# Kernel tuning notes

Hardware: AMD Instinct MI355X
Metric: run time of the kernel (lower is better)

Reference implementation:

```python
import jax, jax.numpy as jnp
import numpy as np

B, S, D, H, FF = 2, 4096, 512, 8, 2048
HD = D // H
EPS = 1e-5


def setup_inputs() -> dict:
    key = jax.random.key(0)
    ks = jax.random.split(key, 14)
    init = lambda k, shape: jax.random.normal(k, shape, dtype=jnp.float32) * 0.02
    return {
        "x": jax.random.normal(ks[0], (B, S, D), dtype=jnp.float32),
        "Wq": init(ks[1], (D, D)), "bq": jnp.zeros((D,), jnp.float32),
        "Wk": init(ks[2], (D, D)), "bk": jnp.zeros((D,), jnp.float32),
        "Wv": init(ks[3], (D, D)), "bv": jnp.zeros((D,), jnp.float32),
        "Wo": init(ks[4], (D, D)), "bo": jnp.zeros((D,), jnp.float32),
        "W1": init(ks[5], (D, FF)), "b1": jnp.zeros((FF,), jnp.float32),
        "W2": init(ks[6], (FF, D)), "b2": jnp.zeros((D,), jnp.float32),
        "g1": jnp.ones((D,), jnp.float32), "beta1": jnp.zeros((D,), jnp.float32),
        "g2": jnp.ones((D,), jnp.float32), "beta2": jnp.zeros((D,), jnp.float32),
    }


def layer_norm(x, g, b):
    mu = jnp.mean(x, axis=-1, keepdims=True)
    var = jnp.mean(jnp.square(x - mu), axis=-1, keepdims=True)
    return (x - mu) * jax.lax.rsqrt(var + EPS) * g + b


def reference(x, Wq, bq, Wk, bk, Wv, bv, Wo, bo, W1, b1, W2, b2, g1, beta1, g2, beta2):
    # --- pre-LN self-attention block ---
    residual = x
    h = layer_norm(x, g1, beta1)
    # project and split heads: [B, H, S, HD]
    q = (h @ Wq + bq).reshape(B, S, H, HD).transpose(0, 2, 1, 3)
    k = (h @ Wk + bk).reshape(B, S, H, HD).transpose(0, 2, 1, 3)
    v = (h @ Wv + bv).reshape(B, S, H, HD).transpose(0, 2, 1, 3)
    scale = HD ** -0.5
    scores = jnp.einsum('bhqd,bhkd->bhqk', q, k) * scale  # [B,H,S,S] materialized
    attn = jax.nn.softmax(scores, axis=-1)
    ctx = jnp.einsum('bhqk,bhkd->bhqd', attn, v)
    ctx = ctx.transpose(0, 2, 1, 3).reshape(B, S, D)
    attn_out = ctx @ Wo + bo
    x = residual + attn_out  # dropout p=0.0 -> identity
    # --- pre-LN FFN block ---
    residual = x
    h = layer_norm(x, g2, beta2)
    h = jax.nn.gelu(h @ W1 + b1, approximate=False)  # nn.GELU default = exact erf
    h = h @ W2 + b2
    x = residual + h
    return (x, attn)
```

## Files before the change

kernel.cpp:

```cpp
#include <hip/hip_runtime.h>
#include <hip/hip_bf16.h>

#define B_ 2
#define S_ 4096
#define D_ 512
#define H_ 8
#define HD_ 64
#define FF_ 2048
#define NT_ (B_*S_)
#define EPS_ 1e-5f

typedef __attribute__((ext_vector_type(8))) short bf16x8;
typedef __attribute__((ext_vector_type(4))) float f32x4;
typedef __attribute__((ext_vector_type(4))) unsigned int u32x4;

__device__ __forceinline__ short f2bf(float f){
  __hip_bfloat16 h = __float2bfloat16(f);
  return __builtin_bit_cast(short, h);
}
__device__ __forceinline__ float bf2f(short s){
  return __bfloat162float(__builtin_bit_cast(__hip_bfloat16, s));
}
__device__ __forceinline__ unsigned pack2(float lo, float hi){
  return ((unsigned)(unsigned short)f2bf(hi) << 16) | (unsigned short)f2bf(lo);
}
__device__ __forceinline__ void load8(const float* p, float* f){
  f32x4 a = *(const f32x4*)p; f32x4 b = *(const f32x4*)(p+4);
  #pragma unroll
  for (int j=0;j<4;j++){ f[j]=a[j]; f[4+j]=b[j]; }
}
__device__ __forceinline__ void load8(const short* p, float* f){
  bf16x8 v = *(const bf16x8*)p;
  #pragma unroll
  for (int j=0;j<8;j++) f[j]=bf2f(v[j]);
}
__device__ __forceinline__ float ldval(const float* p, size_t i){ return p[i]; }
__device__ __forceinline__ float ldval(const short* p, size_t i){ return bf2f(p[i]); }
__device__ __forceinline__ void stval(float* p, size_t i, float v){ p[i]=v; }
__device__ __forceinline__ void stval(short* p, size_t i, float v){ p[i]=f2bf(v); }

#define GLL(src, dst) __builtin_amdgcn_global_load_lds( \
    (const __attribute__((address_space(1))) void*)(src), \
    (__attribute__((address_space(3))) void*)(dst), 16, 0, 0)

__global__ __launch_bounds__(256) void transpose_bf(const float* __restrict__ W,
                                                    short* __restrict__ WT, int K, int N){
  __shared__ float tile[32][33];
  int n0 = blockIdx.x*32, k0 = blockIdx.y*32;
  int tx = threadIdx.x, ty = threadIdx.y;
  #pragma unroll
  for (int i=0;i<32;i+=8)
    tile[ty+i][tx] = W[(size_t)(k0+ty+i)*N + n0+tx];
  __syncthreads();
  #pragma unroll
  for (int i=0;i<32;i+=8)
    WT[(size_t)(n0+ty+i)*K + k0+tx] = f2bf(tile[tx][ty+i]);
}

__global__ __launch_bounds__(256) void transpose_v(const short* __restrict__ V,
                                                   short* __restrict__ VT){
  __shared__ short tile[32][33];
  int d0 = blockIdx.x*32, s0 = blockIdx.y*32, bh = blockIdx.z;
  int b = bh >> 3, h = bh & (H_-1);
  const short* Vp = V + (size_t)b*S_*D_ + (size_t)h*HD_;
  short* VTp = VT + (size_t)bh*HD_*S_;
  int tx = threadIdx.x, ty = threadIdx.y;
  #pragma unroll
  for (int i=0;i<32;i+=8)
    tile[ty+i][tx] = Vp[(size_t)(s0+ty+i)*D_ + d0+tx];
  __syncthreads();
  #pragma unroll
  for (int i=0;i<32;i+=8)
    VTp[(size_t)(d0+ty+i)*S_ + s0+tx] = tile[tx][ty+i];
}

template<typename TIn>
__global__ __launch_bounds__(256) void ln_kernel(const TIn* __restrict__ X,
                                                 const float* __restrict__ G,
                                                 const float* __restrict__ Bt,
                                                 short* __restrict__ O){
  int wid = threadIdx.x>>6, lane = threadIdx.x&63;
  int tok = blockIdx.x*4 + wid;
  const TIn* xp = X + (size_t)tok*D_;
  float f[8]; load8(xp + lane*8, f);
  float s=0.f, s2=0.f;
  #pragma unroll
  for (int j=0;j<8;j++){ s+=f[j]; s2+=f[j]*f[j]; }
  #pragma unroll
  for (int m=1;m<64;m<<=1){ s += __shfl_xor(s,m); s2 += __shfl_xor(s2,m); }
  float mu = s*(1.f/D_);
  float var = s2*(1.f/D_) - mu*mu;
  float rr = rsqrtf(var + EPS_);
  f32x4 g0 = *(const f32x4*)(G + lane*8), g1v = *(const f32x4*)(G + lane*8 + 4);
  f32x4 b0 = *(const f32x4*)(Bt + lane*8), b1v = *(const f32x4*)(Bt + lane*8 + 4);
  bf16x8 o;
  #pragma unroll
  for (int j=0;j<4;j++){
    o[j]   = f2bf((f[j]-mu)*rr*g0[j]  + b0[j]);
    o[4+j] = f2bf((f[4+j]-mu)*rr*g1v[j] + b1v[j]);
  }
  *(bf16x8*)(O + (size_t)tok*D_ + lane*8) = o;
}

template<int EPI, typename TR, typename TO>
__global__ __launch_bounds__(256) void gemm_bt(const short* __restrict__ A,
                                               const short* __restrict__ BT,
                                               const float* __restrict__ bias,
                                               const TR* __restrict__ res,
                                               TO* __restrict__ out,
                                               int M, int N, int K){
  __shared__ short As[128][40];
  __shared__ short Bs[128][40];
  int m0 = blockIdx.y*128, n0 = blockIdx.x*128;
  int tid = threadIdx.x, lane = tid&63, wid = tid>>6;
  int wr = wid>>1, wc = wid&1;
  int r = lane&15, kk = (lane>>4)*8;
  int arow = tid>>2, acol = (tid&3)*8;
  f32x4 zero = {0.f,0.f,0.f,0.f};
  f32x4 acc[4][4];
  #pragma unroll
  for (int i=0;i<4;i++)
    #pragma unroll
    for (int j=0;j<4;j++) acc[i][j] = zero;

  for (int k0=0;k0<K;k0+=32){
    __syncthreads();
    *(bf16x8*)&As[arow][acol]    = *(const bf16x8*)&A [(size_t)(m0+arow)*K    + k0+acol];
    *(bf16x8*)&As[arow+64][acol] = *(const bf16x8*)&A [(size_t)(m0+arow+64)*K + k0+acol];
    *(bf16x8*)&Bs[arow][acol]    = *(const bf16x8*)&BT[(size_t)(n0+arow)*K    + k0+acol];
    *(bf16x8*)&Bs[arow+64][acol] = *(const bf16x8*)&BT[(size_t)(n0+arow+64)*K + k0+acol];
    __syncthreads();
    bf16x8 a[4], b[4];
    #pragma unroll
    for (int i=0;i<4;i++) a[i] = *(const bf16x8*)&As[wr*64+i*16+r][kk];
    #pragma unroll
    for (int i=0;i<4;i++) b[i] = *(const bf16x8*)&Bs[wc*64+i*16+r][kk];
    #pragma unroll
    for (int mi=0;mi<4;mi++)
      #pragma unroll
      for (int ni=0;ni<4;ni++)
        acc[mi][ni] = __builtin_amdgcn_mfma_f32_16x16x32_bf16(a[mi], b[ni], acc[mi][ni], 0,0,0);
  }
  #pragma unroll
  for (int mi=0;mi<4;mi++){
    #pragma unroll
    for (int ni=0;ni<4;ni++){
      int col = n0 + wc*64 + ni*16 + r;
      float bs = bias[col];
      #pragma unroll
      for (int j=0;j<4;j++){
        int row = m0 + wr*64 + mi*16 + (lane>>4)*4 + j;
        float v = acc[mi][ni][j] + bs;
        if (EPI==1) v += ldval(res, (size_t)row*N + col);
        if (EPI==2) v = 0.5f*v*(1.f + erff(v*0.70710678118f));
        stval(out, (size_t)row*N + col, v);
      }
    }
  }
}

__global__ __launch_bounds__(256, 2) void attn_kernel(const short* __restrict__ Q,
                                                      const short* __restrict__ Kt,
                                                      const short* __restrict__ VT,
                                                      float* __restrict__ attn_o,
                                                      short* __restrict__ ctx){
  __shared__ __align__(16) char smem[65536];
  __shared__ float dcomb[4][4][16];
  int wid = threadIdx.x>>6, lane = threadIdx.x&63;
  int bh = blockIdx.y, b = bh>>3, h = bh&7;
  int q0 = blockIdx.x*64;
  int koff = wid*1024;
  int r = lane&15, qh = lane>>4;
  bool hi4 = (lane>>4)&1, hi5 = (lane>>5)&1;
  const short* Qp = Q  + (size_t)b*S_*D_ + (size_t)h*HD_;
  const short* Kp = Kt + (size_t)b*S_*D_ + (size_t)h*HD_;
  const short* Vp = VT + (size_t)bh*HD_*S_;
  float* Ap = attn_o + (size_t)bh*S_*S_;

  char* stg = smem + wid*16384;
  short* KB0 = (short*)stg;         short* KB1 = (short*)(stg+4096);
  short* VB0 = (short*)(stg+8192);  short* VB1 = (short*)(stg+12288);

  auto stageK = [&](int sc, short* buf){
    #pragma unroll
    for (int i=0;i<4;i++){
      int row = i*8 + (lane>>3);
      int col = ((lane&7)*8) ^ ((row&7)*8);
      GLL(&Kp[(size_t)(sc+row)*D_ + col], buf + i*512);
    }
  };
  auto stageV = [&](int sc, short* buf){
    #pragma unroll
    for (int i=0;i<4;i++){
      int d = i*16 + (lane>>2);
      int col = ((lane&3)*8) ^ ((d&3)*8);
      GLL(&Vp[(size_t)d*S_ + sc + col], buf + i*512);
    }
  };
  const int kc0 = (qh*16) ^ ((r&7)<<4);
  const int kc1 = (64 + qh*16) ^ ((r&7)<<4);
  const int vc  = (qh*16) ^ ((r&3)<<4);

  bf16x8 aq[4][2];
  #pragma unroll
  for (int qt=0;qt<4;qt++){
    aq[qt][0] = *(const bf16x8*)&Qp[(size_t)(q0+qt*16+r)*D_ + qh*8];
    aq[qt][1] = *(const bf16x8*)&Qp[(size_t)(q0+qt*16+r)*D_ + 32 + qh*8];
  }
  const f32x4 zero = {0.f,0.f,0.f,0.f};

  float part[4] = {0.f,0.f,0.f,0.f};

#define S1BODY(n, NW, DOSTG) { \
  asm volatile("s_waitcnt vmcnt(" #NW ")" ::: "memory"); \
  short* kb_ = ((n)&1)? KB1 : KB0; \
  bf16x8 kf0 = *(const bf16x8*)((char*)kb_ + r*128 + kc0); \
  bf16x8 kf1 = *(const bf16x8*)((char*)kb_ + r*128 + kc1); \
  bf16x8 kf2 = *(const bf16x8*)((char*)kb_ + (16+r)*128 + kc0); \
  bf16x8 kf3 = *(const bf16x8*)((char*)kb_ + (16+r)*128 + kc1); \
  asm volatile("s_waitcnt lgkmcnt(0)" ::: "memory"); \
  if (DOSTG) stageK(koff + ((n)+2)*32, kb_); \
  _Pragma("unroll") \
  for (int qt=0;qt<4;qt++){ \
    f32x4 s0 = __builtin_amdgcn_mfma_f32_16x16x32_bf16(kf0, aq[qt][0], zero, 0,0,0); \
    s0 = __builtin_amdgcn_mfma_f32_16x16x32_bf16(kf1, aq[qt][1], s0, 0,0,0); \
    f32x4 s1 = __builtin_amdgcn_mfma_f32_16x16x32_bf16(kf2, aq[qt][0], zero, 0,0,0); \
    s1 = __builtin_amdgcn_mfma_f32_16x16x32_bf16(kf3, aq[qt][1], s1, 0,0,0); \
    _Pragma("unroll") \
    for (int j=0;j<4;j++) part[qt] += __expf(s0[j]*0.125f) + __expf(s1[j]*0.125f); \
  } \
}

  stageK(koff, KB0); stageK(koff+32, KB1);
  S1BODY(0,4,1)
  for (int k2=0;k2<14;k2++){ S1BODY(2*k2+1,4,1) S1BODY(2*k2+2,4,1) }
  S1BODY(29,4,1) S1BODY(30,4,0) S1BODY(31,0,0)

  #pragma unroll
  for (int qt=0;qt<4;qt++){
    part[qt] += __shfl_xor(part[qt],16);
    part[qt] += __shfl_xor(part[qt],32);
  }
  if (lane < 16){
    #pragma unroll
    for (int qt=0;qt<4;qt++) dcomb[wid][qt][r] = part[qt];
  }
  __syncthreads();
  float invl[4];
  #pragma unroll
  for (int qt=0;qt<4;qt++)
    invl[qt] = 1.f/(dcomb[0][qt][r]+dcomb[1][qt][r]+dcomb[2][qt][r]+dcomb[3][qt][r]);

  f32x4 cacc[4][4];
  #pragma unroll
  for (int qt=0;qt<4;qt++)
    #pragma unroll
    for (int n2=0;n2<4;n2++) cacc[qt][n2] = zero;

#define S2BODY(n, NW, DOSTG) { \
  asm volatile("s_waitcnt vmcnt(" #NW ")" ::: "memory"); \
  short* kb_ = ((n)&1)? KB1 : KB0; \
  short* vb_ = ((n)&1)? VB1 : VB0; \
  int sc_ = koff + (n)*32; \
  bf16x8 kf0 = *(const bf16x8*)((char*)kb_ + r*128 + kc0); \
  bf16x8 kf1 = *(const bf16x8*)((char*)kb_ + r*128 + kc1); \
  bf16x8 kf2 = *(const bf16x8*)((char*)kb_ + (16+r)*128 + kc0); \
  bf16x8 kf3 = *(const bf16x8*)((char*)kb_ + (16+r)*128 + kc1); \
  bf16x8 vf0 = *(const bf16x8*)((char*)vb_ + (r)*64    + vc); \
  bf16x8 vf1 = *(const bf16x8*)((char*)vb_ + (16+r)*64 + vc); \
  bf16x8 vf2 = *(const bf16x8*)((char*)vb_ + (32+r)*64 + vc); \
  bf16x8 vf3 = *(const bf16x8*)((char*)vb_ + (48+r)*64 + vc); \
  asm volatile("s_waitcnt lgkmcnt(0)" ::: "memory"); \
  if (DOSTG){ stageK(koff+((n)+2)*32, kb_); stageV(koff+((n)+2)*32, vb_); } \
  _Pragma("unroll") \
  for (int qt=0;qt<4;qt++){ \
    f32x4 s0 = __builtin_amdgcn_mfma_f32_16x16x32_bf16(kf0, aq[qt][0], zero, 0,0,0); \
    s0 = __builtin_amdgcn_mfma_f32_16x16x32_bf16(kf1, aq[qt][1], s0, 0,0,0); \
    f32x4 s1 = __builtin_amdgcn_mfma_f32_16x16x32_bf16(kf2, aq[qt][0], zero, 0,0,0); \
    s1 = __builtin_amdgcn_mfma_f32_16x16x32_bf16(kf3, aq[qt][1], s1, 0,0,0); \
    float e0[4], e1[4]; \
    _Pragma("unroll") \
    for (int j=0;j<4;j++){ \
      e0[j] = __expf(s0[j]*0.125f)*invl[qt]; \
      e1[j] = __expf(s1[j]*0.125f)*invl[qt]; \
    } \
    f32x4 o0 = {e0[0],e0[1],e0[2],e0[3]}; \
    f32x4 o1 = {e1[0],e1[1],e1[2],e1[3]}; \
    float* dst = &Ap[(size_t)(q0+qt*16+r)*S_ + sc_ + qh*4]; \
    *(f32x4*)dst = o0; \
    *(f32x4*)(dst+16) = o1; \
    unsigned v0 = pack2(e0[0],e0[1]), v1 = pack2(e0[2],e0[3]); \
    unsigned v2 = pack2(e1[0],e1[1]), v3 = pack2(e1[2],e1[3]); \
    unsigned u0 = __shfl_xor((int)v0,16), u1 = __shfl_xor((int)v1,16); \
    unsigned u2 = __shfl_xor((int)v2,16), u3 = __shfl_xor((int)v3,16); \
    unsigned s0c0 = hi4?u0:v0, s0c1 = hi4?u1:v1, s0c2 = hi4?v0:u0, s0c3 = hi4?v1:u1; \
    unsigned s1c0 = hi4?u2:v2, s1c1 = hi4?u3:v3, s1c2 = hi4?v2:u2, s1c3 = hi4?v3:u3; \
    unsigned w0 = hi5?s0c0:s1c0, w1 = hi5?s0c1:s1c1, w2 = hi5?s0c2:s1c2, w3 = hi5?s0c3:s1c3; \
    unsigned wp0 = __shfl_xor((int)w0,32), wp1 = __shfl_xor((int)w1,32); \
    unsigned wp2 = __shfl_xor((int)w2,32), wp3 = __shfl_xor((int)w3,32); \
    u32x4 pw; \
    pw[0] = (qh==0)?s0c0:(qh==3)?s1c0:wp0; \
    pw[1] = (qh==0)?s0c1:(qh==3)?s1c1:wp1; \
    pw[2] = (qh==0)?s0c2:(qh==3)?s1c2:wp2; \
    pw[3] = (qh==0)?s0c3:(qh==3)?s1c3:wp3; \
    bf16x8 pa = __builtin_bit_cast(bf16x8, pw); \
    cacc[qt][0] = __builtin_amdgcn_mfma_f32_16x16x32_bf16(pa, vf0, cacc[qt][0], 0,0,0); \
    cacc[qt][1] = __builtin_amdgcn_mfma_f32_16x16x32_bf16(pa, vf1, cacc[qt][1], 0,0,0); \
    cacc[qt][2] = __builtin_amdgcn_mfma_f32_16x16x32_bf16(pa, vf2, cacc[qt][2], 0,0,0); \
    cacc[qt][3] = __builtin_amdgcn_mfma_f32_16x16x32_bf16(pa, vf3, cacc[qt][3], 0,0,0); \
  } \
}

  stageK(koff, KB0); stageV(koff, VB0);
  stageK(koff+32, KB1); stageV(koff+32, VB1);
  S2BODY(0,8,1)
  for (int k2=0;k2<14;k2++){ S2BODY(2*k2+1,16,1) S2BODY(2*k2+2,16,1) }
  S2BODY(29,16,1) S2BODY(30,16,0) S2BODY(31,8,0)

  __syncthreads();
  float* cmb = (float*)smem;
  if (wid & 1){
    float* dstp = cmb + (wid>>1)*4096;
    #pragma unroll
    for (int qt=0;qt<4;qt++)
      #pragma unroll
      for (int n2=0;n2<4;n2++)
        #pragma unroll
        for (int j=0;j<4;j++)
          dstp[(qt*16+qh*4+j)*64 + n2*16 + r] = cacc[qt][n2][j];
  }
  __syncthreads();
  if (!(wid & 1)){
    float* srcp = cmb + (wid>>1)*4096;
    #pragma unroll
    for (int qt=0;qt<4;qt++)
      #pragma unroll
      for (int n2=0;n2<4;n2++)
        #pragma unroll
        for (int j=0;j<4;j++)
          cacc[qt][n2][j] += srcp[(qt*16+qh*4+j)*64 + n2*16 + r];
  }
  __syncthreads();
  if (wid == 2){
    #pragma unroll
    for (int qt=0;qt<4;qt++)
      #pragma unroll
      for (int n2=0;n2<4;n2++)
        #pragma unroll
        for (int j=0;j<4;j++)
          cmb[(qt*16+qh*4+j)*64 + n2*16 + r] = cacc[qt][n2][j];
  }
  __syncthreads();
  if (wid == 0){
    #pragma unroll
    for (int qt=0;qt<4;qt++)
      #pragma unroll
      for (int n2=0;n2<4;n2++)
        #pragma unroll
        for (int j=0;j<4;j++){
          float v = cacc[qt][n2][j] + cmb[(qt*16+qh*4+j)*64 + n2*16 + r];
          ctx[(size_t)(b*S_ + q0 + qt*16 + qh*4 + j)*D_ + h*HD_ + n2*16 + r] = f2bf(v);
        }
  }
}

extern "C" void kernel_launch(void* const* d_in, const int* in_sizes, int n_in,
                              void* d_out, int out_size, void* d_ws, size_t ws_size,
                              hipStream_t stream){
  const float* x   = (const float*)d_in[0];
  const float* Wq  = (const float*)d_in[1];
  const float* bq  = (const float*)d_in[2];
  const float* Wk  = (const float*)d_in[3];
  const float* bk  = (const float*)d_in[4];
  const float* Wv  = (const float*)d_in[5];
  const float* bv  = (const float*)d_in[6];
  const float* Wo  = (const float*)d_in[7];
  const float* bo  = (const float*)d_in[8];
  const float* W1  = (const float*)d_in[9];
  const float* b1  = (const float*)d_in[10];
  const float* W2  = (const float*)d_in[11];
  const float* b2  = (const float*)d_in[12];
  const float* g1  = (const float*)d_in[13];
  const float* be1 = (const float*)d_in[14];
  const float* g2  = (const float*)d_in[15];
  const float* be2 = (const float*)d_in[16];

  char* ws = (char*)d_ws;
  const size_t KB = 1024;
  short* wqT = (short*)(ws + 0*KB);
  short* wkT = (short*)(ws + 512*KB);
  short* wvT = (short*)(ws + 1024*KB);
  short* woT = (short*)(ws + 1536*KB);
  short* w1T = (short*)(ws + 2048*KB);
  short* w2T = (short*)(ws + 4096*KB);
  short* hbf = (short*)(ws + 6144*KB);
  short* Qb  = (short*)(ws + 14336*KB);
  short* Kb  = (short*)(ws + 22528*KB);
  short* Vb  = (short*)(ws + 30720*KB);
  short* VTb = (short*)(ws + 38912*KB);
  short* ctx = (short*)(ws + 47104*KB);
  short* f1  = (short*)(ws + 14336*KB);

  float* out0 = (float*)d_out;
  float* attn = out0 + (size_t)NT_*D_;

  dim3 tb(32,8);
  transpose_bf<<<dim3(16,16),tb,0,stream>>>(Wq, wqT, 512, 512);
  transpose_bf<<<dim3(16,16),tb,0,stream>>>(Wk, wkT, 512, 512);
  transpose_bf<<<dim3(16,16),tb,0,stream>>>(Wv, wvT, 512, 512);
  transpose_bf<<<dim3(16,16),tb,0,stream>>>(Wo, woT, 512, 512);
  transpose_bf<<<dim3(64,16),tb,0,stream>>>(W1, w1T, 512, 2048);
  transpose_bf<<<dim3(16,64),tb,0,stream>>>(W2, w2T, 2048, 512);

  ln_kernel<float><<<NT_/4, 256, 0, stream>>>(x, g1, be1, hbf);

  gemm_bt<0,float,short><<<dim3(4,64),256,0,stream>>>(hbf, wqT, bq, nullptr, Qb, NT_, 512, 512);
  gemm_bt<0,float,short><<<dim3(4,64),256,0,stream>>>(hbf, wkT, bk, nullptr, Kb, NT_, 512, 512);
  gemm_bt<0,float,short><<<dim3(4,64),256,0,stream>>>(hbf, wvT, bv, nullptr, Vb, NT_, 512, 512);

  transpose_v<<<dim3(2,128,16),tb,0,stream>>>(Vb, VTb);

  attn_kernel<<<dim3(64,16), 256, 0, stream>>>(Qb, Kb, VTb, attn, ctx);

  gemm_bt<1,float,float><<<dim3(4,64),256,0,stream>>>(ctx, woT, bo, x, out0, NT_, 512, 512);

  ln_kernel<float><<<NT_/4, 256, 0, stream>>>(out0, g2, be2, hbf);

  gemm_bt<2,float,short><<<dim3(16,64),256,0,stream>>>(hbf, w1T, b1, nullptr, f1, NT_, 2048, 512);

  gemm_bt<1,float,float><<<dim3(4,64),256,0,stream>>>(f1, w2T, b2, out0, out0, NT_, 512, 2048);
}
```

Measured before the change: 578.5 us.

## Split attention into denominator and output kernels; use direct-to-LDS swizzled GEMM loads

```diff
diff --git a/kernel.cpp b/kernel.cpp
--- a/kernel.cpp
+++ b/kernel.cpp
@@ -109,13 +109,14 @@
                                                const TR* __restrict__ res,
                                                TO* __restrict__ out,
                                                int M, int N, int K){
-  __shared__ short As[128][40];
-  __shared__ short Bs[128][40];
+  __shared__ __align__(16) short As[128*64];
+  __shared__ __align__(16) short Bs[128*64];
   int m0 = blockIdx.y*128, n0 = blockIdx.x*128;
   int tid = threadIdx.x, lane = tid&63, wid = tid>>6;
   int wr = wid>>1, wc = wid&1;
-  int r = lane&15, kk = (lane>>4)*8;
-  int arow = tid>>2, acol = (tid&3)*8;
+  int r = lane&15, qh = lane>>4;
+  int srow = wid*32 + (lane>>3);
+  int scole = ((lane&7)*8);
   f32x4 zero = {0.f,0.f,0.f,0.f};
   f32x4 acc[4][4];
   #pragma unroll
@@ -123,23 +124,32 @@
     #pragma unroll
     for (int j=0;j<4;j++) acc[i][j] = zero;
 
-  for (int k0=0;k0<K;k0+=32){
+  for (int k0=0;k0<K;k0+=64){
     __syncthreads();
-    *(bf16x8*)&As[arow][acol]    = *(const bf16x8*)&A [(size_t)(m0+arow)*K    + k0+acol];
-    *(bf16x8*)&As[arow+64][acol] = *(const bf16x8*)&A [(size_t)(m0+arow+64)*K + k0+acol];
-    *(bf16x8*)&Bs[arow][acol]    = *(const bf16x8*)&BT[(size_t)(n0+arow)*K    + k0+acol];
-    *(bf16x8*)&Bs[arow+64][acol] = *(const bf16x8*)&BT[(size_t)(n0+arow+64)*K + k0+acol];
+    #pragma unroll
+    for (int i=0;i<4;i++){
+      int row = srow + i*8;
+      int cole = scole ^ ((row&7)*8);
+      GLL(&A [(size_t)(m0+row)*K + k0 + cole], As + (size_t)(wid*32+i*8)*64);
+      GLL(&BT[(size_t)(n0+row)*K + k0 + cole], Bs + (size_t)(wid*32+i*8)*64);
+    }
     __syncthreads();
-    bf16x8 a[4], b[4];
-    #pragma unroll
-    for (int i=0;i<4;i++) a[i] = *(const bf16x8*)&As[wr*64+i*16+r][kk];
-    #pragma unroll
-    for (int i=0;i<4;i++) b[i] = *(const bf16x8*)&Bs[wc*64+i*16+r][kk];
-    #pragma unroll
-    for (int mi=0;mi<4;mi++)
-      #pragma unroll
-      for (int ni=0;ni<4;ni++)
-        acc[mi][ni] = __builtin_amdgcn_mfma_f32_16x16x32_bf16(a[mi], b[ni], acc[mi][ni], 0,0,0);
+    #pragma unroll
+    for (int half=0; half<2; half++){
+      bf16x8 a[4], b[4];
+      #pragma unroll
+      for (int i=0;i<4;i++){
+        int ar = wr*64+i*16+r;
+        a[i] = *(const bf16x8*)((const char*)As + (size_t)ar*128 + ((qh*16+half*64) ^ ((ar&7)*16)));
+        int br = wc*64+i*16+r;
+        b[i] = *(const bf16x8*)((const char*)Bs + (size_t)br*128 + ((qh*16+half*64) ^ ((br&7)*16)));
+      }
+      #pragma unroll
+      for (int mi=0;mi<4;mi++)
+        #pragma unroll
+        for (int ni=0;ni<4;ni++)
+          acc[mi][ni] = __builtin_amdgcn_mfma_f32_16x16x32_bf16(a[mi], b[ni], acc[mi][ni], 0,0,0);
+    }
   }
   #pragma unroll
   for (int mi=0;mi<4;mi++){
@@ -159,27 +169,21 @@
   }
 }
 
-__global__ __launch_bounds__(256, 2) void attn_kernel(const short* __restrict__ Q,
-                                                      const short* __restrict__ Kt,
-                                                      const short* __restrict__ VT,
-                                                      float* __restrict__ attn_o,
-                                                      short* __restrict__ ctx){
-  __shared__ __align__(16) char smem[65536];
+__global__ __launch_bounds__(256, 4) void attn_s1(const short* __restrict__ Q,
+                                                  const short* __restrict__ Kt,
+                                                  float* __restrict__ dinv){
+  __shared__ __align__(16) char smem[32768];
   __shared__ float dcomb[4][4][16];
   int wid = threadIdx.x>>6, lane = threadIdx.x&63;
   int bh = blockIdx.y, b = bh>>3, h = bh&7;
   int q0 = blockIdx.x*64;
   int koff = wid*1024;
   int r = lane&15, qh = lane>>4;
-  bool hi4 = (lane>>4)&1, hi5 = (lane>>5)&1;
   const short* Qp = Q  + (size_t)b*S_*D_ + (size_t)h*HD_;
   const short* Kp = Kt + (size_t)b*S_*D_ + (size_t)h*HD_;
-  const short* Vp = VT + (size_t)bh*HD_*S_;
-  float* Ap = attn_o + (size_t)bh*S_*S_;
-
-  char* stg = smem + wid*16384;
-  short* KB0 = (short*)stg;         short* KB1 = (short*)(stg+4096);
-  short* VB0 = (short*)(stg+8192);  short* VB1 = (short*)(stg+12288);
+
+  char* stg = smem + wid*8192;
+  short* KB0 = (short*)stg;  short* KB1 = (short*)(stg+4096);
 
   auto stageK = [&](int sc, short* buf){
     #pragma unroll
@@ -189,17 +193,8 @@
       GLL(&Kp[(size_t)(sc+row)*D_ + col], buf + i*512);
     }
   };
-  auto stageV = [&](int sc, short* buf){
-    #pragma unroll
-    for (int i=0;i<4;i++){
-      int d = i*16 + (lane>>2);
-      int col = ((lane&3)*8) ^ ((d&3)*8);
-      GLL(&Vp[(size_t)d*S_ + sc + col], buf + i*512);
-    }
-  };
   const int kc0 = (qh*16) ^ ((r&7)<<4);
   const int kc1 = (64 + qh*16) ^ ((r&7)<<4);
-  const int vc  = (qh*16) ^ ((r&3)<<4);
 
   bf16x8 aq[4][2];
   #pragma unroll
@@ -208,7 +203,6 @@
     aq[qt][1] = *(const bf16x8*)&Qp[(size_t)(q0+qt*16+r)*D_ + 32 + qh*8];
   }
   const f32x4 zero = {0.f,0.f,0.f,0.f};
-
   float part[4] = {0.f,0.f,0.f,0.f};
 
 #define S1BODY(n, NW, DOSTG) { \
@@ -235,6 +229,7 @@
   S1BODY(0,4,1)
   for (int k2=0;k2<14;k2++){ S1BODY(2*k2+1,4,1) S1BODY(2*k2+2,4,1) }
   S1BODY(29,4,1) S1BODY(30,4,0) S1BODY(31,0,0)
+#undef S1BODY
 
   #pragma unroll
   for (int qt=0;qt<4;qt++){
@@ -246,10 +241,66 @@
     for (int qt=0;qt<4;qt++) dcomb[wid][qt][r] = part[qt];
   }
   __syncthreads();
+  if (wid == 0){
+    int qt = lane>>4, rr = lane&15;
+    float s = dcomb[0][qt][rr]+dcomb[1][qt][rr]+dcomb[2][qt][rr]+dcomb[3][qt][rr];
+    dinv[(size_t)bh*S_ + q0 + qt*16 + rr] = 1.f/s;
+  }
+}
+
+__global__ __launch_bounds__(256, 2) void attn_s2(const short* __restrict__ Q,
+                                                  const short* __restrict__ Kt,
+                                                  const short* __restrict__ VT,
+                                                  const float* __restrict__ dinv,
+                                                  float* __restrict__ attn_o,
+                                                  short* __restrict__ ctx){
+  __shared__ __align__(16) char smem[65536];
+  int wid = threadIdx.x>>6, lane = threadIdx.x&63;
+  int bh = blockIdx.y, b = bh>>3, h = bh&7;
+  int q0 = blockIdx.x*64;
+  int koff = wid*1024;
+  int r = lane&15, qh = lane>>4;
+  bool hi4 = (lane>>4)&1, hi5 = (lane>>5)&1;
+  const short* Qp = Q  + (size_t)b*S_*D_ + (size_t)h*HD_;
+  const short* Kp = Kt + (size_t)b*S_*D_ + (size_t)h*HD_;
+  const short* Vp = VT + (size_t)bh*HD_*S_;
+  float* Ap = attn_o + (size_t)bh*S_*S_;
+
+  char* stg = smem + wid*16384;
+  short* KB0 = (short*)stg;         short* KB1 = (short*)(stg+4096);
+  short* VB0 = (short*)(stg+8192);  short* VB1 = (short*)(stg+12288);
+
+  auto stageK = [&](int sc, short* buf){
+    #pragma unroll
+    for (int i=0;i<4;i++){
+      int row = i*8 + (lane>>3);
+      int col = ((lane&7)*8) ^ ((row&7)*8);
+      GLL(&Kp[(size_t)(sc+row)*D_ + col], buf + i*512);
+    }
+  };
+  auto stageV = [&](int sc, short* buf){
+    #pragma unroll
+    for (int i=0;i<4;i++){
+      int d = i*16 + (lane>>2);
+      int col = ((lane&3)*8) ^ ((d&3)*8);
+      GLL(&Vp[(size_t)d*S_ + sc + col], buf + i*512);
+    }
+  };
+  const int kc0 = (qh*16) ^ ((r&7)<<4);
+  const int kc1 = (64 + qh*16) ^ ((r&7)<<4);
+  const int vc  = (qh*16) ^ ((r&3)<<4);
+
   float invl[4];
   #pragma unroll
-  for (int qt=0;qt<4;qt++)
-    invl[qt] = 1.f/(dcomb[0][qt][r]+dcomb[1][qt][r]+dcomb[2][qt][r]+dcomb[3][qt][r]);
+  for (int qt=0;qt<4;qt++) invl[qt] = dinv[(size_t)bh*S_ + q0 + qt*16 + r];
+
+  bf16x8 aq[4][2];
+  #pragma unroll
+  for (int qt=0;qt<4;qt++){
+    aq[qt][0] = *(const bf16x8*)&Qp[(size_t)(q0+qt*16+r)*D_ + qh*8];
+    aq[qt][1] = *(const bf16x8*)&Qp[(size_t)(q0+qt*16+r)*D_ + 32 + qh*8];
+  }
+  const f32x4 zero = {0.f,0.f,0.f,0.f};
 
   f32x4 cacc[4][4];
   #pragma unroll
@@ -316,6 +367,7 @@
   S2BODY(0,8,1)
   for (int k2=0;k2<14;k2++){ S2BODY(2*k2+1,16,1) S2BODY(2*k2+2,16,1) }
   S2BODY(29,16,1) S2BODY(30,16,0) S2BODY(31,8,0)
+#undef S2BODY
 
   __syncthreads();
   float* cmb = (float*)smem;
@@ -399,6 +451,7 @@
   short* Vb  = (short*)(ws + 30720*KB);
   short* VTb = (short*)(ws + 38912*KB);
   short* ctx = (short*)(ws + 47104*KB);
+  float* dinv= (float*)(ws + 55296*KB);
   short* f1  = (short*)(ws + 14336*KB);
 
   float* out0 = (float*)d_out;
@@ -420,7 +473,8 @@
 
   transpose_v<<<dim3(2,128,16),tb,0,stream>>>(Vb, VTb);
 
-  attn_kernel<<<dim3(64,16), 256, 0, stream>>>(Qb, Kb, VTb, attn, ctx);
+  attn_s1<<<dim3(64,16), 256, 0, stream>>>(Qb, Kb, dinv);
+  attn_s2<<<dim3(64,16), 256, 0, stream>>>(Qb, Kb, VTb, dinv, attn, ctx);
 
   gemm_bt<1,float,float><<<dim3(4,64),256,0,stream>>>(ctx, woT, bo, x, out0, NT_, 512, 512);
 
```

Result: slower. 598.0 us (+3.4%).
